# Optimization experiments

Hardware: AMD Instinct MI355X
Metric: run time of the kernel (lower is better)

Reference implementation:

```python
import jax, jax.numpy as jnp
import numpy as np

EPS = 1e-07


def setup_inputs() -> dict:
    key = jax.random.key(0)
    k1, k2, k3 = jax.random.split(key, 3)
    N, D, E = 100000, 128, 600000
    z = jax.random.normal(k1, (N, D), dtype=jnp.float32)
    edge_index = jax.random.randint(k2, (2, E), 0, N, dtype=jnp.int64)
    W = jax.random.normal(k3, (D,), dtype=jnp.float32) * (1.0 / np.sqrt(D))
    b = jnp.zeros((), dtype=jnp.float32)
    return {"z": z, "edge_index": edge_index, "W": W, "b": b}


def reference(z, edge_index, W, b):
    src = edge_index[0]
    dst = edge_index[1]
    z_i = z[src]                      # [E, D]
    z_j = z[dst]                      # [E, D]
    m_j = z_j @ W + b                 # [E]  (Linear(D,1).squeeze(-1))
    diff = z_i - z_j
    dist2 = jnp.sum(diff * diff, axis=-1) + EPS   # [E]
    log_d = jnp.log(dist2)
    logits = m_j - log_d
    prob = jax.nn.sigmoid(logits)
    return (logits, prob, m_j, dist2)
```

## Files before the change

### kernel.cpp

```cpp
#include <hip/hip_runtime.h>
#include <hip/hip_fp16.h>
#include <math.h>

#define D 128
#define EPS 1e-7f

typedef _Float16 half2v __attribute__((ext_vector_type(2)));
typedef unsigned int uint;

__device__ __forceinline__ float dot2acc(half2v a, half2v b, float c) {
#if __has_builtin(__builtin_amdgcn_fdot2)
    return __builtin_amdgcn_fdot2(a, b, c, false);
#else
    return c + (float)a.x * (float)b.x + (float)a.y * (float)b.y;
#endif
}

__device__ __forceinline__ float d2_of(uint x, uint y, float acc) {
    half2v d = __builtin_bit_cast(half2v, x) - __builtin_bit_cast(half2v, y);
    return dot2acc(d, d, acc);
}

__global__ __launch_bounds__(256) void node_precompute_kernel(
    const float* __restrict__ z, const float* __restrict__ W,
    const float* __restrict__ b,
    _Float16* __restrict__ zh, float* __restrict__ m, int N)
{
    const int lane = threadIdx.x & 63;
    const int half = lane >> 5, sub = lane & 31;
    const int n = (blockIdx.x * (blockDim.x >> 6) + (threadIdx.x >> 6)) * 2 + half;
    if (n >= N) return;

    const float4 a = ((const float4*)(z + (size_t)n * D))[sub];
    const float4 w = ((const float4*)W)[sub];
    float dot = a.x * w.x + a.y * w.y + a.z * w.z + a.w * w.w;
    #pragma unroll
    for (int off = 16; off > 0; off >>= 1) dot += __shfl_xor(dot, off);

    half2v h0 = { (_Float16)a.x, (_Float16)a.y };
    half2v h1 = { (_Float16)a.z, (_Float16)a.w };
    uint2 pack;
    pack.x = __builtin_bit_cast(uint, h0);
    pack.y = __builtin_bit_cast(uint, h1);
    ((uint2*)(zh + (size_t)n * D))[sub] = pack;

    if (sub == 0) m[n] = dot + b[0];
}

__global__ __launch_bounds__(256) void edge_kernel(
    const _Float16* __restrict__ zh, const float* __restrict__ m,
    const int* __restrict__ ei, float* __restrict__ out, int E)
{
    const int lane = threadIdx.x & 63;
    const int sub = lane & 7;
    const int e = (blockIdx.x * (blockDim.x >> 6) + (threadIdx.x >> 6)) * 8
                  + (lane >> 3);
    if (e >= E) return;

    const int src = ei[e];
    const int dst = ei[E + e];
    const float mj = m[dst];

    const uint4* ri = (const uint4*)(zh + (size_t)src * D) + sub * 2;
    const uint4* rj = (const uint4*)(zh + (size_t)dst * D) + sub * 2;
    const uint4 a0 = ri[0];
    const uint4 a1 = ri[1];
    const uint4 c0 = rj[0];
    const uint4 c1 = rj[1];

    float d2 = 0.f;
    d2 = d2_of(a0.x, c0.x, d2);
    d2 = d2_of(a0.y, c0.y, d2);
    d2 = d2_of(a0.z, c0.z, d2);
    d2 = d2_of(a0.w, c0.w, d2);
    d2 = d2_of(a1.x, c1.x, d2);
    d2 = d2_of(a1.y, c1.y, d2);
    d2 = d2_of(a1.z, c1.z, d2);
    d2 = d2_of(a1.w, c1.w, d2);

    #pragma unroll
    for (int off = 4; off > 0; off >>= 1) d2 += __shfl_xor(d2, off);

    if (sub == 0) {
        const float dist2  = d2 + EPS;
        const float logits = mj - __logf(dist2);
        const float prob   = 1.0f / (1.0f + __expf(-logits));
        out[e]         = logits;
        out[E + e]     = prob;
        out[2 * E + e] = mj;
        out[3 * E + e] = dist2;
    }
}

__global__ __launch_bounds__(256) void gravity_decoder_fallback(
    const float* __restrict__ z, const int* __restrict__ ei,
    const float* __restrict__ W, const float* __restrict__ b,
    float* __restrict__ out, int E)
{
    const int lane = threadIdx.x & 63;
    const int half = lane >> 5, sub = lane & 31;
    const int e = (blockIdx.x * (blockDim.x >> 6) + (threadIdx.x >> 6)) * 2 + half;
    if (e >= E) return;
    const int src = ei[e], dst = ei[E + e];
    const float4* z4 = (const float4*)z;
    const float4 a = z4[(size_t)src * (D / 4) + sub];
    const float4 c = z4[(size_t)dst * (D / 4) + sub];
    const float4 w = ((const float4*)W)[sub];
    float dot = c.x * w.x + c.y * w.y + c.z * w.z + c.w * w.w;
    const float dx = a.x - c.x, dy = a.y - c.y, dz = a.z - c.z, dw = a.w - c.w;
    float d2 = dx * dx + dy * dy + dz * dz + dw * dw;
    #pragma unroll
    for (int off = 16; off > 0; off >>= 1) {
        dot += __shfl_xor(dot, off);
        d2  += __shfl_xor(d2,  off);
    }
    if (sub == 0) {
        const float mj = dot + b[0];
        const float dist2 = d2 + EPS;
        const float logits = mj - __logf(dist2);
        const float prob = 1.0f / (1.0f + __expf(-logits));
        out[e] = logits; out[E + e] = prob;
        out[2 * E + e] = mj; out[3 * E + e] = dist2;
    }
}

extern "C" void kernel_launch(void* const* d_in, const int* in_sizes, int n_in,
                              void* d_out, int out_size, void* d_ws, size_t ws_size,
                              hipStream_t stream)
{
    const float* z  = (const float*)d_in[0];
    const int*   ei = (const int*)d_in[1];
    const float* W  = (const float*)d_in[2];
    const float* b  = (const float*)d_in[3];
    float* out = (float*)d_out;

    const int E = in_sizes[1] / 2;
    const int N = in_sizes[0] / D;

    const size_t zh_bytes = (size_t)N * D * sizeof(_Float16);
    const size_t m_bytes  = (size_t)N * sizeof(float);

    if (ws_size >= zh_bytes + m_bytes) {
        _Float16* zh = (_Float16*)d_ws;
        float*    m  = (float*)((char*)d_ws + zh_bytes);

        const int nodes_per_block = 8;
        node_precompute_kernel<<<(N + nodes_per_block - 1) / nodes_per_block,
                                 256, 0, stream>>>(z, W, b, zh, m, N);

        const int edges_per_block = 32;
        edge_kernel<<<(E + edges_per_block - 1) / edges_per_block,
                      256, 0, stream>>>(zh, m, ei, out, E);
    } else {
        const int edges_per_block = 8;
        gravity_decoder_fallback<<<(E + edges_per_block - 1) / edges_per_block,
                                   256, 0, stream>>>(z, ei, W, b, out, E);
    }
}
```

Measured before the change: 134.1 us.

## Quantize node embeddings to int8 and compute distance via dot-product expansion

The node precompute now quantizes each row of z to int8 with a per-row scale and stores a per-node metadata float4 holding the scale, the squared norm of the quantized row, and m. The edge kernel gathers 128-byte int8 rows instead of 256-byte fp16 rows, computes an integer dot product with sdot4, and rebuilds dist2 as |a|^2 + |b|^2 - 2a·b. This halves gather traffic per edge. In exchange, int8 quantization together with the norm-expansion form can cause cancellation error when the two nodes are close, which may break accuracy tolerances on dist2 and log(dist2).

```diff
diff --git a/kernel.cpp b/kernel.cpp
--- a/kernel.cpp
+++ b/kernel.cpp
@@ -5,26 +5,28 @@
 #define D 128
 #define EPS 1e-7f
 
-typedef _Float16 half2v __attribute__((ext_vector_type(2)));
 typedef unsigned int uint;
 
-__device__ __forceinline__ float dot2acc(half2v a, half2v b, float c) {
-#if __has_builtin(__builtin_amdgcn_fdot2)
-    return __builtin_amdgcn_fdot2(a, b, c, false);
+__device__ __forceinline__ int sdot4(int a, int b, int c) {
+#if __has_builtin(__builtin_amdgcn_sdot4)
+    return __builtin_amdgcn_sdot4(a, b, c, false);
 #else
-    return c + (float)a.x * (float)b.x + (float)a.y * (float)b.y;
+    int r = c;
+    #pragma unroll
+    for (int i = 0; i < 4; ++i) {
+        int av = (a << (24 - 8 * i)) >> 24;
+        int bv = (b << (24 - 8 * i)) >> 24;
+        r += av * bv;
+    }
+    return r;
 #endif
-}
-
-__device__ __forceinline__ float d2_of(uint x, uint y, float acc) {
-    half2v d = __builtin_bit_cast(half2v, x) - __builtin_bit_cast(half2v, y);
-    return dot2acc(d, d, acc);
 }
 
 __global__ __launch_bounds__(256) void node_precompute_kernel(
     const float* __restrict__ z, const float* __restrict__ W,
     const float* __restrict__ b,
-    _Float16* __restrict__ zh, float* __restrict__ m, int N)
+    uint* __restrict__ zq,
+    float4* __restrict__ meta, int N)
 {
     const int lane = threadIdx.x & 63;
     const int half = lane >> 5, sub = lane & 31;
@@ -33,22 +35,42 @@
 
     const float4 a = ((const float4*)(z + (size_t)n * D))[sub];
     const float4 w = ((const float4*)W)[sub];
+
     float dot = a.x * w.x + a.y * w.y + a.z * w.z + a.w * w.w;
+    float amax = fmaxf(fmaxf(fabsf(a.x), fabsf(a.y)), fmaxf(fabsf(a.z), fabsf(a.w)));
     #pragma unroll
-    for (int off = 16; off > 0; off >>= 1) dot += __shfl_xor(dot, off);
+    for (int off = 16; off > 0; off >>= 1) {
+        dot  += __shfl_xor(dot, off);
+        amax  = fmaxf(amax, __shfl_xor(amax, off));
+    }
 
-    half2v h0 = { (_Float16)a.x, (_Float16)a.y };
-    half2v h1 = { (_Float16)a.z, (_Float16)a.w };
-    uint2 pack;
-    pack.x = __builtin_bit_cast(uint, h0);
-    pack.y = __builtin_bit_cast(uint, h1);
-    ((uint2*)(zh + (size_t)n * D))[sub] = pack;
+    const float s   = amax * (1.0f / 127.0f);
+    const float inv = 127.0f / fmaxf(amax, 1e-30f);
 
-    if (sub == 0) m[n] = dot + b[0];
+    const int q0 = (int)rintf(fminf(fmaxf(a.x * inv, -127.f), 127.f));
+    const int q1 = (int)rintf(fminf(fmaxf(a.y * inv, -127.f), 127.f));
+    const int q2 = (int)rintf(fminf(fmaxf(a.z * inv, -127.f), 127.f));
+    const int q3 = (int)rintf(fminf(fmaxf(a.w * inv, -127.f), 127.f));
+    const uint pack = (uint)(q0 & 255) | ((uint)(q1 & 255) << 8)
+                    | ((uint)(q2 & 255) << 16) | ((uint)q3 << 24);
+    zq[(size_t)n * 32 + sub] = pack;
+
+    int S = sdot4((int)pack, (int)pack, 0);
+    #pragma unroll
+    for (int off = 16; off > 0; off >>= 1) S += __shfl_xor(S, off);
+
+    if (sub == 0) {
+        float4 mt;
+        mt.x = s;
+        mt.y = __builtin_bit_cast(float, S);
+        mt.z = dot + b[0];
+        mt.w = 0.f;
+        meta[n] = mt;
+    }
 }
 
 __global__ __launch_bounds__(256) void edge_kernel(
-    const _Float16* __restrict__ zh, const float* __restrict__ m,
+    const uint* __restrict__ zq, const float4* __restrict__ meta,
     const int* __restrict__ ei, float* __restrict__ out, int E)
 {
     const int lane = threadIdx.x & 63;
@@ -59,30 +81,32 @@
 
     const int src = ei[e];
     const int dst = ei[E + e];
-    const float mj = m[dst];
 
-    const uint4* ri = (const uint4*)(zh + (size_t)src * D) + sub * 2;
-    const uint4* rj = (const uint4*)(zh + (size_t)dst * D) + sub * 2;
-    const uint4 a0 = ri[0];
-    const uint4 a1 = ri[1];
-    const uint4 c0 = rj[0];
-    const uint4 c1 = rj[1];
+    const float4 Mi = meta[src];
+    const float4 Mj = meta[dst];
 
-    float d2 = 0.f;
-    d2 = d2_of(a0.x, c0.x, d2);
-    d2 = d2_of(a0.y, c0.y, d2);
-    d2 = d2_of(a0.z, c0.z, d2);
-    d2 = d2_of(a0.w, c0.w, d2);
-    d2 = d2_of(a1.x, c1.x, d2);
-    d2 = d2_of(a1.y, c1.y, d2);
-    d2 = d2_of(a1.z, c1.z, d2);
-    d2 = d2_of(a1.w, c1.w, d2);
+    const uint4 ai = ((const uint4*)(zq + (size_t)src * 32))[sub];
+    const uint4 ci = ((const uint4*)(zq + (size_t)dst * 32))[sub];
+
+    int dot = sdot4((int)ai.x, (int)ci.x, 0);
+    dot = sdot4((int)ai.y, (int)ci.y, dot);
+    dot = sdot4((int)ai.z, (int)ci.z, dot);
+    dot = sdot4((int)ai.w, (int)ci.w, dot);
 
     #pragma unroll
-    for (int off = 4; off > 0; off >>= 1) d2 += __shfl_xor(d2, off);
+    for (int off = 4; off > 0; off >>= 1) dot += __shfl_xor(dot, off);
 
     if (sub == 0) {
-        const float dist2  = d2 + EPS;
+        const float si = Mi.x, sj = Mj.x;
+        const int   Si = __builtin_bit_cast(int, Mi.y);
+        const int   Sj = __builtin_bit_cast(int, Mj.y);
+        const float mj = Mj.z;
+
+        const float u = (si * si) * (float)Si;
+        const float v = (sj * sj) * (float)Sj;
+        const float wc = (si * sj) * (float)dot;
+        const float dist2 = fmaxf(u + v - wc - wc, 0.0f) + EPS;
+
         const float logits = mj - __logf(dist2);
         const float prob   = 1.0f / (1.0f + __expf(-logits));
         out[e]         = logits;
@@ -137,20 +161,20 @@
     const int E = in_sizes[1] / 2;
     const int N = in_sizes[0] / D;
 
-    const size_t zh_bytes = (size_t)N * D * sizeof(_Float16);
-    const size_t m_bytes  = (size_t)N * sizeof(float);
+    const size_t zq_bytes   = (size_t)N * D;
+    const size_t meta_bytes = (size_t)N * sizeof(float4);
 
-    if (ws_size >= zh_bytes + m_bytes) {
-        _Float16* zh = (_Float16*)d_ws;
-        float*    m  = (float*)((char*)d_ws + zh_bytes);
+    if (ws_size >= zq_bytes + meta_bytes) {
+        uint*   zq   = (uint*)d_ws;
+        float4* meta = (float4*)((char*)d_ws + zq_bytes);
 
         const int nodes_per_block = 8;
         node_precompute_kernel<<<(N + nodes_per_block - 1) / nodes_per_block,
-                                 256, 0, stream>>>(z, W, b, zh, m, N);
+                                 256, 0, stream>>>(z, W, b, zq, meta, N);
 
         const int edges_per_block = 32;
         edge_kernel<<<(E + edges_per_block - 1) / edges_per_block,
-                      256, 0, stream>>>(zh, m, ei, out, E);
+                      256, 0, stream>>>(zq, meta, ei, out, E);
     } else {
         const int edges_per_block = 8;
         gravity_decoder_fallback<<<(E + edges_per_block - 1) / edges_per_block,
```

Result: faster. 119.9 us (-10.6%).
